# Performance work log

Measured on AMD Instinct MI355X. Metric: run time of the kernel, lower is better.

The kernel has to match this reference:

```python
import jax, jax.numpy as jnp
import numpy as np

N_NODES = 100000


def _sage_conv(x, src, dst, W_l, W_r, b):
    # mean aggregation of neighbor features over incoming edges (src -> dst)
    msgs = x[src]                                            # [E, d] gather
    agg = jax.ops.segment_sum(msgs, dst, num_segments=N_NODES)
    deg = jax.ops.segment_sum(jnp.ones_like(dst, dtype=x.dtype), dst,
                              num_segments=N_NODES)
    mean = agg / jnp.maximum(deg, 1.0)[:, None]              # [N, d]
    # PyG SAGEConv: lin_l(aggr) + lin_r(x); bias lives in lin_l
    return mean @ W_l + x @ W_r + b


def setup_inputs() -> dict:
    key = jax.random.key(0)
    k = jax.random.split(key, 8)
    d_in, d_h, E = 128, 128, 1600000
    scale_in = 1.0 / np.sqrt(d_in)
    scale_h = 1.0 / np.sqrt(d_h)
    return {
        "x": jax.random.normal(k[0], (N_NODES, d_in), dtype=jnp.float32),
        "edge_index": jax.random.randint(k[1], (2, E), 0, N_NODES, dtype=jnp.int64),
        "W_l0": jax.random.uniform(k[2], (d_in, d_h), jnp.float32, -scale_in, scale_in),
        "W_r0": jax.random.uniform(k[3], (d_in, d_h), jnp.float32, -scale_in, scale_in),
        "b0": jnp.zeros((d_h,), jnp.float32),
        "W_l1": jax.random.uniform(k[4], (d_h, d_h), jnp.float32, -scale_h, scale_h),
        "W_r1": jax.random.uniform(k[5], (d_h, d_h), jnp.float32, -scale_h, scale_h),
        "b1": jnp.zeros((d_h,), jnp.float32),
    }


def reference(x, edge_index, W_l0, W_r0, b0, W_l1, W_r1, b1):
    src, dst = edge_index[0], edge_index[1]
    h = _sage_conv(x, src, dst, W_l0, W_r0, b0)
    h = jax.nn.relu(h)  # dropout p=0.0 / eval mode -> identity
    h = _sage_conv(h, src, dst, W_l1, W_r1, b1)
    return h
```

## Files before the change

kernel.cpp:

```cpp
#include <hip/hip_runtime.h>


using bf16x8 = __attribute__((ext_vector_type(8))) __bf16;
using f32x4  = __attribute__((ext_vector_type(4))) float;
using f32x2  = __attribute__((ext_vector_type(2))) float;

__device__ __forceinline__ unsigned short f2bf(float f) {
    __bf16 b = (__bf16)f;
    return __builtin_bit_cast(unsigned short, b);
}
__device__ __forceinline__ unsigned pk2(float a, float b) {
    return (unsigned)f2bf(a) | ((unsigned)f2bf(b) << 16);
}

__device__ __forceinline__ int exscan1024(int v, int* wsum, int t) {
    int lane = t & 63, w = t >> 6;
    int x = v;
#pragma unroll
    for (int s = 1; s < 64; s <<= 1) {
        int y = __shfl_up(x, s);
        if (lane >= s) x += y;
    }
    if (lane == 63) wsum[w] = x;
    __syncthreads();
    if (w == 0) {
        int ws = (lane < 16) ? wsum[lane] : 0;
#pragma unroll
        for (int s = 1; s < 16; s <<= 1) {
            int y = __shfl_up(ws, s);
            if (lane >= s) ws += y;
        }
        if (lane < 16) wsum[lane] = ws;
    }
    __syncthreads();
    int base = (w > 0) ? wsum[w - 1] : 0;
    return base + x - v;
}


__global__ __launch_bounds__(256) void k_prep(
    const float4* __restrict__ x, uint4* __restrict__ xb8, int nvec, int ncvt,
    const float* __restrict__ W0, const float* __restrict__ W1,
    const float* __restrict__ W2, const float* __restrict__ W3,
    unsigned short* __restrict__ wsw, int ncvtw,
    const int* __restrict__ dst, int E, int* __restrict__ ghist, int nb, int nhist,
    int* __restrict__ gbase, int* __restrict__ gcur,
    int* __restrict__ row_start, int n)
{
    __shared__ int lh[800];
    const int b = blockIdx.x;
    if (b < ncvt) {
        int i = b * 256 + threadIdx.x;
        if (i >= nvec) return;
        float4 a = x[2 * i], c = x[2 * i + 1];
        uint4 o;
        o.x = pk2(a.x, a.y);
        o.y = pk2(a.z, a.w);
        o.z = pk2(c.x, c.y);
        o.w = pk2(c.z, c.w);
        xb8[i] = o;
    } else if (b < ncvt + ncvtw) {
        int id = (b - ncvt) * 256 + threadIdx.x;
        int m = id >> 14, r = id & 16383;
        int c = r >> 7, k = r & 127;
        const float* W = (m == 0) ? W0 : (m == 1) ? W1 : (m == 2) ? W2 : W3;
        wsw[m * 16384 + c * 128 + (k ^ ((c & 7) << 3))] = f2bf(W[k * 128 + c]);
    } else {
        int hb = b - ncvt - ncvtw;
        for (int i = threadIdx.x; i < nb; i += 256) lh[i] = 0;
        __syncthreads();
        for (int e = hb * 256 + threadIdx.x; e < E; e += nhist * 256)
            atomicAdd(&lh[dst[e] >> 7], 1);
        __syncthreads();
        for (int i = threadIdx.x; i < nb; i += 256)
            if (lh[i]) atomicAdd(&ghist[i], lh[i]);

        __shared__ int winflag;
        __shared__ int swsum[4];
        if (threadIdx.x == 0) {
            __threadfence();
            winflag = (atomicAdd(&ghist[nb], 1) == nhist - 1) ? 1 : 0;
        }
        __syncthreads();
        if (!winflag) return;
        __threadfence();

        const int t = threadIdx.x, lane = t & 63, w = t >> 6;
        const int i0 = t * 4;
        int v0 = (i0 + 0 < nb) ? __hip_atomic_load(&ghist[i0 + 0], __ATOMIC_RELAXED, __HIP_MEMORY_SCOPE_AGENT) : 0;
        int v1 = (i0 + 1 < nb) ? __hip_atomic_load(&ghist[i0 + 1], __ATOMIC_RELAXED, __HIP_MEMORY_SCOPE_AGENT) : 0;
        int v2 = (i0 + 2 < nb) ? __hip_atomic_load(&ghist[i0 + 2], __ATOMIC_RELAXED, __HIP_MEMORY_SCOPE_AGENT) : 0;
        int v3 = (i0 + 3 < nb) ? __hip_atomic_load(&ghist[i0 + 3], __ATOMIC_RELAXED, __HIP_MEMORY_SCOPE_AGENT) : 0;
        int s = v0 + v1 + v2 + v3;
        int xx = s;
#pragma unroll
        for (int sh = 1; sh < 64; sh <<= 1) {
            int y = __shfl_up(xx, sh);
            if (lane >= sh) xx += y;
        }
        if (lane == 63) swsum[w] = xx;
        __syncthreads();
        int base = 0;
        if (w > 0) base += swsum[0];
        if (w > 1) base += swsum[1];
        if (w > 2) base += swsum[2];
        int run = base + xx - s;
        if (i0 + 0 < nb) { gbase[i0 + 0] = run; gcur[i0 + 0] = run; } run += v0;
        if (i0 + 1 < nb) { gbase[i0 + 1] = run; gcur[i0 + 1] = run; } run += v1;
        if (i0 + 2 < nb) { gbase[i0 + 2] = run; gcur[i0 + 2] = run; } run += v2;
        if (i0 + 3 < nb) { gbase[i0 + 3] = run; gcur[i0 + 3] = run; }
        if (t == 0) { gbase[nb] = E; row_start[n] = E; }
    }
}


#define SC_CHUNK 8192

__global__ __launch_bounds__(1024) void k_binscatter(const int* __restrict__ src,
                                                     const int* __restrict__ dst, int E,
                                                     int* __restrict__ gcur,
                                                     unsigned* __restrict__ binned, int nb)
{
    __shared__ int lh[800];
    __shared__ int lbase[800];
    __shared__ int gb[800];
    __shared__ int wsum[16];
    __shared__ unsigned long long staged[SC_CHUNK];
    int t = threadIdx.x;
    int e0 = blockIdx.x * SC_CHUNK;
    if (e0 >= E) return;
    int ecnt = E - e0; if (ecnt > SC_CHUNK) ecnt = SC_CHUNK;

    for (int i = t; i < nb; i += 1024) lh[i] = 0;
    __syncthreads();
    for (int i = t; i < ecnt; i += 1024)
        atomicAdd(&lh[dst[e0 + i] >> 7], 1);
    __syncthreads();
    int v = (t < nb) ? lh[t] : 0;
    int excl = exscan1024(v, wsum, t);
    if (t < nb) {
        lbase[t] = excl;
        gb[t] = v ? atomicAdd(&gcur[t], v) : 0;
        lh[t] = excl;
    }
    __syncthreads();
    for (int i = t; i < ecnt; i += 1024) {
        int d = dst[e0 + i], s = src[e0 + i];
        int b = d >> 7;
        int rank = atomicAdd(&lh[b], 1);
        unsigned pack = ((unsigned)s << 7) | (unsigned)(d & 127);
        unsigned gaddr = (unsigned)gb[b] + (unsigned)(rank - lbase[b]);
        staged[rank] = ((unsigned long long)gaddr << 32) | pack;
    }
    __syncthreads();
    for (int i = t; i < ecnt; i += 1024) {
        unsigned long long w = staged[i];
        binned[(unsigned)(w >> 32)] = (unsigned)w;
    }
}


#define BS_STAGE 8192

__global__ __launch_bounds__(256) void k_bucketsort(
    const unsigned* __restrict__ binned,
    const int* __restrict__ gbase,
    int* __restrict__ csr,
    int* __restrict__ row_start,
    float* __restrict__ inv_deg,
    int n)
{
    __shared__ int cnt[128];
    __shared__ int cur[128];
    __shared__ int wsum[4];
    __shared__ unsigned stg[BS_STAGE];
    const int t = threadIdx.x;
    const int b = blockIdx.x;
    const int beg = gbase[b], end = gbase[b + 1];
    const int len = end - beg;

    if (t < 128) cnt[t] = 0;
    __syncthreads();
    for (int i = beg + t; i < end; i += 256)
        atomicAdd(&cnt[binned[i] & 127], 1);
    __syncthreads();
    int v = (t < 128) ? cnt[t] : 0;
    {
        int lane = t & 63, w = t >> 6;
        int x = v;
#pragma unroll
        for (int s = 1; s < 64; s <<= 1) {
            int y = __shfl_up(x, s);
            if (lane >= s) x += y;
        }
        if (lane == 63) wsum[w] = x;
        __syncthreads();
        int base = (w == 1) ? wsum[0] : (w == 2) ? wsum[0] + wsum[1]
                 : (w == 3) ? wsum[0] + wsum[1] + wsum[2] : 0;
        int excl = base + x - v;
        if (t < 128) {
            cur[t] = excl;
            int node = b * 128 + t;
            if (node < n) {
                row_start[node] = beg + excl;
                inv_deg[node] = 1.f / (float)max(v, 1);
            }
        }
    }
    __syncthreads();

    if (len <= BS_STAGE) {
        for (int i = beg + t; i < end; i += 256) {
            unsigned w = binned[i];
            int r = atomicAdd(&cur[w & 127], 1);
            stg[r] = w >> 7;
        }
        __syncthreads();
        for (int i = t; i < len; i += 256)
            csr[beg + i] = (int)stg[i];
    } else {
        for (int i = beg + t; i < end; i += 256) {
            unsigned w = binned[i];
            int r = atomicAdd(&cur[w & 127], 1);
            csr[beg + r] = (int)(w >> 7);
        }
    }
}


__device__ __forceinline__ f32x2 up2(unsigned x) {
    return (f32x2){__builtin_bit_cast(float, x << 16),
                   __builtin_bit_cast(float, x & 0xffff0000u)};
}
__device__ __forceinline__ void acc8(f32x2* a, uint4 v) {
    a[0] += up2(v.x);
    a[1] += up2(v.y);
    a[2] += up2(v.z);
    a[3] += up2(v.w);
}

__global__ __launch_bounds__(256) void k_agg(
    const unsigned short* __restrict__ feat,
    const int* __restrict__ csr,
    const int* __restrict__ row_start,
    const float* __restrict__ inv_deg,
    unsigned short* __restrict__ mean, int n)
{
    const int node = blockIdx.x * 4 + (threadIdx.x >> 6);
    if (node >= n) return;
    const int lane = threadIdx.x & 63;
    const int q  = lane >> 4;
    const int cg = (lane & 15) << 3;
    const unsigned short* fp = feat + cg;
    const int beg = row_start[node], end = row_start[node + 1];

    f32x2 a[4];
#pragma unroll
    for (int j = 0; j < 4; ++j) a[j] = (f32x2){0.f, 0.f};

    for (int i = beg; i < end; i += 64) {
        int cnt = end - i; if (cnt > 64) cnt = 64;
        const int lim = i + cnt - 1;
        for (int e = 0; e < cnt; e += 16) {
            int p0 = i + e + q;      p0 = p0 < lim ? p0 : lim;
            int p1 = i + e + 4 + q;  p1 = p1 < lim ? p1 : lim;
            int p2 = i + e + 8 + q;  p2 = p2 < lim ? p2 : lim;
            int p3 = i + e + 12 + q; p3 = p3 < lim ? p3 : lim;
            int s0 = csr[p0];
            int s1 = csr[p1];
            int s2 = csr[p2];
            int s3 = csr[p3];
            uint4 v0 = *(const uint4*)(fp + ((size_t)s0 << 7));
            uint4 v1 = *(const uint4*)(fp + ((size_t)s1 << 7));
            uint4 v2 = *(const uint4*)(fp + ((size_t)s2 << 7));
            uint4 v3 = *(const uint4*)(fp + ((size_t)s3 << 7));
            if (e + q      < cnt) acc8(a, v0);
            if (e + 4 + q  < cnt) acc8(a, v1);
            if (e + 8 + q  < cnt) acc8(a, v2);
            if (e + 12 + q < cnt) acc8(a, v3);
        }
    }

#pragma unroll
    for (int j = 0; j < 4; ++j) {
        a[j].x += __shfl_xor(a[j].x, 16);
        a[j].x += __shfl_xor(a[j].x, 32);
        a[j].y += __shfl_xor(a[j].y, 16);
        a[j].y += __shfl_xor(a[j].y, 32);
    }

    if (q == 0) {
        float w = inv_deg[node];
        uint4 o;
        o.x = pk2(a[0].x * w, a[0].y * w);
        o.y = pk2(a[1].x * w, a[1].y * w);
        o.z = pk2(a[2].x * w, a[2].y * w);
        o.w = pk2(a[3].x * w, a[3].y * w);
        *(uint4*)(mean + (size_t)node * 128 + cg) = o;
    }
}


template<bool RELU, bool OUTF32>
__global__ __launch_bounds__(256) void k_gemm(
    const unsigned short* __restrict__ A1,
    const unsigned short* __restrict__ A2,
    const unsigned short* __restrict__ Wsw,
    const float* __restrict__ bias,
    void* __restrict__ outv,
    int nrows)
{
    __shared__ __align__(16) unsigned short Wt[2 * 128 * 128];
    {
        const uint4* wsrc = (const uint4*)Wsw;
        uint4* wdst = (uint4*)Wt;
#pragma unroll
        for (int i = 0; i < 16; ++i)
            wdst[threadIdx.x + 256 * i] = wsrc[threadIdx.x + 256 * i];
    }
    __syncthreads();

    const int lane = threadIdx.x & 63;
    const int wave = threadIdx.x >> 6;
    const int lr = lane & 15;
    const int lg = lane >> 4;
    const int row0 = blockIdx.x * 128 + wave * 32;
    const int sw = (lr & 7) << 3;

    f32x4 acc[2][8];
#pragma unroll
    for (int m = 0; m < 2; ++m)
#pragma unroll
        for (int nn = 0; nn < 8; ++nn) acc[m][nn] = (f32x4){0.f, 0.f, 0.f, 0.f};

#pragma unroll
    for (int ks = 0; ks < 4; ++ks) {
        const int k0 = ks * 32 + lg * 8;
        bf16x8 a1[2], a2[2];
#pragma unroll
        for (int m = 0; m < 2; ++m) {
            int r = row0 + m * 16 + lr;
            if (r >= nrows) r = nrows - 1;
            a1[m] = *reinterpret_cast<const bf16x8*>(A1 + (size_t)r * 128 + k0);
            a2[m] = *reinterpret_cast<const bf16x8*>(A2 + (size_t)r * 128 + k0);
        }
        const int kidx = k0 ^ sw;
#pragma unroll
        for (int nn = 0; nn < 8; ++nn) {
            const int c = nn * 16 + lr;
            bf16x8 b1 = *reinterpret_cast<const bf16x8*>(&Wt[c * 128 + kidx]);
            bf16x8 b2 = *reinterpret_cast<const bf16x8*>(&Wt[16384 + c * 128 + kidx]);
#pragma unroll
            for (int m = 0; m < 2; ++m) {
                acc[m][nn] = __builtin_amdgcn_mfma_f32_16x16x32_bf16(a1[m], b1, acc[m][nn], 0, 0, 0);
                acc[m][nn] = __builtin_amdgcn_mfma_f32_16x16x32_bf16(a2[m], b2, acc[m][nn], 0, 0, 0);
            }
        }
    }

    __syncthreads();

#pragma unroll
    for (int m = 0; m < 2; ++m) {
#pragma unroll
        for (int nn = 0; nn < 8; ++nn) {
            const int c = nn * 16 + lr;
            const float bv = bias[c];
#pragma unroll
            for (int i = 0; i < 4; ++i) {
                int r = row0 + m * 16 + lg * 4 + i;
                if (r < nrows) {
                    float v = acc[m][nn][i] + bv;
                    if (RELU) v = fmaxf(v, 0.f);
                    if (OUTF32)
                        ((float*)outv)[(size_t)r * 128 + c] = v;
                    else
                        ((unsigned short*)outv)[(size_t)r * 128 + c] = f2bf(v);
                }
            }
        }
    }
}


extern "C" void kernel_launch(void* const* d_in, const int* in_sizes, int n_in,
                              void* d_out, int out_size, void* d_ws, size_t ws_size,
                              hipStream_t stream)
{
    const float* x   = (const float*)d_in[0];
    const int*   ei  = (const int*)d_in[1];
    const float* Wl0 = (const float*)d_in[2];
    const float* Wr0 = (const float*)d_in[3];
    const float* b0  = (const float*)d_in[4];
    const float* Wl1 = (const float*)d_in[5];
    const float* Wr1 = (const float*)d_in[6];
    const float* b1  = (const float*)d_in[7];
    float* out = (float*)d_out;

    const int n = in_sizes[0] / 128;
    const int E = in_sizes[1] / 2;
    const int* src = ei;
    const int* dst = ei + E;
    const int nb = (n + 127) >> 7;

    char* ws = (char*)d_ws;
    size_t off = 0;
    auto alloc = [&](size_t sz) -> char* {
        char* p = ws + off;
        off += (sz + 1023) & ~(size_t)1023;
        return p;
    };
    unsigned short* xb     = (unsigned short*)alloc((size_t)n * 128 * 2);
    unsigned short* mean   = (unsigned short*)alloc((size_t)n * 128 * 2);
    unsigned*       binned = (unsigned*)      alloc((size_t)E * 4);
    int*            rs     = (int*)           alloc((size_t)(n + 1) * 4);
    float*          invd   = (float*)         alloc((size_t)n * 4);
    int*            ghist  = (int*)           alloc((size_t)(nb + 1) * 4);
    int*            gbase  = (int*)           alloc((size_t)(nb + 1) * 4);
    int*            gcur   = (int*)           alloc((size_t)nb * 4);
    unsigned short* wsw    = (unsigned short*)alloc(4 * 16384 * 2);
    int* csr;
    if (off + (size_t)E * 4 <= ws_size) csr = (int*)alloc((size_t)E * 4);
    else                                csr = (int*)binned;
    if (ws_size < off) return;

    const int nvec  = n * 128 / 8;
    const int ncvt  = (nvec + 255) / 256;
    const int ncvtw = 256;
    const int nhist = 512;
    const int nsc   = (E + SC_CHUNK - 1) / SC_CHUNK;

    hipMemsetAsync(ghist, 0, (size_t)(nb + 1) * sizeof(int), stream);
    hipLaunchKernelGGL(k_prep, dim3(ncvt + ncvtw + nhist), dim3(256), 0, stream,
                       (const float4*)x, (uint4*)xb, nvec, ncvt,
                       Wl0, Wr0, Wl1, Wr1, wsw, ncvtw,
                       dst, E, ghist, nb, nhist,
                       gbase, gcur, rs, n);
    hipLaunchKernelGGL(k_binscatter, dim3(nsc),  dim3(1024), 0, stream,
                       src, dst, E, gcur, binned, nb);
    hipLaunchKernelGGL(k_bucketsort, dim3(nb),   dim3(256),  0, stream,
                       binned, gbase, csr, rs, invd, n);
    hipLaunchKernelGGL(k_agg,  dim3((n + 3) / 4), dim3(256), 0, stream,
                       xb, csr, rs, invd, mean, n);
    hipLaunchKernelGGL((k_gemm<true, false>), dim3(nb), dim3(256), 0, stream,
                       mean, xb, wsw, b0, (void*)xb, n);
    hipLaunchKernelGGL(k_agg,  dim3((n + 3) / 4), dim3(256), 0, stream,
                       xb, csr, rs, invd, mean, n);
    hipLaunchKernelGGL((k_gemm<false, true>), dim3(nb), dim3(256), 0, stream,
                       mean, xb, wsw + 2 * 16384, b1, (void*)out, n);
}
```

Measured before the change: 235.9 us.

## Fuse neighbor mean aggregation with SAGE GEMM per 128-node block

Merges the aggregation and GEMM kernels into one: each block aggregates 128 nodes into a swizzled LDS tile, then runs the MFMA GEMM straight from LDS. This drops the global round trip of the mean buffer and two launches. Edge indices are now loaded once per 64-edge chunk and broadcast with shuffles, and the weights are read from global/L2 instead of being staged in LDS. The cost is far fewer blocks for the gather phase (782 blocks of 4 waves, each wave walking 32 nodes one after another), which may hurt latency hiding. The layer-1 output also moves to a separate buffer.

```diff
diff --git a/kernel.cpp b/kernel.cpp
--- a/kernel.cpp
+++ b/kernel.cpp
@@ -239,93 +239,79 @@
     a[3] += up2(v.w);
 }
 
-__global__ __launch_bounds__(256) void k_agg(
+template<bool RELU, bool OUTF32>
+__global__ __launch_bounds__(256) void k_fused(
     const unsigned short* __restrict__ feat,
     const int* __restrict__ csr,
     const int* __restrict__ row_start,
     const float* __restrict__ inv_deg,
-    unsigned short* __restrict__ mean, int n)
-{
-    const int node = blockIdx.x * 4 + (threadIdx.x >> 6);
-    if (node >= n) return;
-    const int lane = threadIdx.x & 63;
-    const int q  = lane >> 4;
-    const int cg = (lane & 15) << 3;
-    const unsigned short* fp = feat + cg;
-    const int beg = row_start[node], end = row_start[node + 1];
-
-    f32x2 a[4];
-#pragma unroll
-    for (int j = 0; j < 4; ++j) a[j] = (f32x2){0.f, 0.f};
-
-    for (int i = beg; i < end; i += 64) {
-        int cnt = end - i; if (cnt > 64) cnt = 64;
-        const int lim = i + cnt - 1;
-        for (int e = 0; e < cnt; e += 16) {
-            int p0 = i + e + q;      p0 = p0 < lim ? p0 : lim;
-            int p1 = i + e + 4 + q;  p1 = p1 < lim ? p1 : lim;
-            int p2 = i + e + 8 + q;  p2 = p2 < lim ? p2 : lim;
-            int p3 = i + e + 12 + q; p3 = p3 < lim ? p3 : lim;
-            int s0 = csr[p0];
-            int s1 = csr[p1];
-            int s2 = csr[p2];
-            int s3 = csr[p3];
-            uint4 v0 = *(const uint4*)(fp + ((size_t)s0 << 7));
-            uint4 v1 = *(const uint4*)(fp + ((size_t)s1 << 7));
-            uint4 v2 = *(const uint4*)(fp + ((size_t)s2 << 7));
-            uint4 v3 = *(const uint4*)(fp + ((size_t)s3 << 7));
-            if (e + q      < cnt) acc8(a, v0);
-            if (e + 4 + q  < cnt) acc8(a, v1);
-            if (e + 8 + q  < cnt) acc8(a, v2);
-            if (e + 12 + q < cnt) acc8(a, v3);
-        }
-    }
-
-#pragma unroll
-    for (int j = 0; j < 4; ++j) {
-        a[j].x += __shfl_xor(a[j].x, 16);
-        a[j].x += __shfl_xor(a[j].x, 32);
-        a[j].y += __shfl_xor(a[j].y, 16);
-        a[j].y += __shfl_xor(a[j].y, 32);
-    }
-
-    if (q == 0) {
-        float w = inv_deg[node];
-        uint4 o;
-        o.x = pk2(a[0].x * w, a[0].y * w);
-        o.y = pk2(a[1].x * w, a[1].y * w);
-        o.z = pk2(a[2].x * w, a[2].y * w);
-        o.w = pk2(a[3].x * w, a[3].y * w);
-        *(uint4*)(mean + (size_t)node * 128 + cg) = o;
-    }
-}
-
-
-template<bool RELU, bool OUTF32>
-__global__ __launch_bounds__(256) void k_gemm(
-    const unsigned short* __restrict__ A1,
-    const unsigned short* __restrict__ A2,
     const unsigned short* __restrict__ Wsw,
     const float* __restrict__ bias,
     void* __restrict__ outv,
-    int nrows)
+    int n)
 {
-    __shared__ __align__(16) unsigned short Wt[2 * 128 * 128];
-    {
-        const uint4* wsrc = (const uint4*)Wsw;
-        uint4* wdst = (uint4*)Wt;
-#pragma unroll
-        for (int i = 0; i < 16; ++i)
-            wdst[threadIdx.x + 256 * i] = wsrc[threadIdx.x + 256 * i];
-    }
-    __syncthreads();
-
+    __shared__ __align__(16) unsigned short Ml[128 * 128];
     const int lane = threadIdx.x & 63;
     const int wave = threadIdx.x >> 6;
+    const int node0 = blockIdx.x * 128;
+
+    {
+        const int q  = lane >> 4;
+        const int cg = (lane & 15) << 3;
+        const unsigned short* fp = feat + cg;
+        for (int j = 0; j < 32; ++j) {
+            const int nl = wave * 32 + j;
+            const int node = node0 + nl;
+            f32x2 a[4];
+#pragma unroll
+            for (int k = 0; k < 4; ++k) a[k] = (f32x2){0.f, 0.f};
+            if (node < n) {
+                const int beg = row_start[node], end = row_start[node + 1];
+                for (int i = beg; i < end; i += 64) {
+                    int cnt = end - i; if (cnt > 64) cnt = 64;
+                    int idx = csr[i + (lane < cnt ? lane : cnt - 1)];
+                    for (int e = 0; e < cnt; e += 16) {
+                        const int r0 = e + q, r1 = e + 4 + q,
+                                  r2 = e + 8 + q, r3 = e + 12 + q;
+                        int s0 = __shfl(idx, r0 < cnt ? r0 : cnt - 1);
+                        int s1 = __shfl(idx, r1 < cnt ? r1 : cnt - 1);
+                        int s2 = __shfl(idx, r2 < cnt ? r2 : cnt - 1);
+                        int s3 = __shfl(idx, r3 < cnt ? r3 : cnt - 1);
+                        uint4 v0 = *(const uint4*)(fp + ((size_t)s0 << 7));
+                        uint4 v1 = *(const uint4*)(fp + ((size_t)s1 << 7));
+                        uint4 v2 = *(const uint4*)(fp + ((size_t)s2 << 7));
+                        uint4 v3 = *(const uint4*)(fp + ((size_t)s3 << 7));
+                        if (r0 < cnt) acc8(a, v0);
+                        if (r1 < cnt) acc8(a, v1);
+                        if (r2 < cnt) acc8(a, v2);
+                        if (r3 < cnt) acc8(a, v3);
+                    }
+                }
+            }
+#pragma unroll
+            for (int k = 0; k < 4; ++k) {
+                a[k].x += __shfl_xor(a[k].x, 16);
+                a[k].x += __shfl_xor(a[k].x, 32);
+                a[k].y += __shfl_xor(a[k].y, 16);
+                a[k].y += __shfl_xor(a[k].y, 32);
+            }
+            if (q == 0) {
+                float w = (node < n) ? inv_deg[node] : 0.f;
+                uint4 o;
+                o.x = pk2(a[0].x * w, a[0].y * w);
+                o.y = pk2(a[1].x * w, a[1].y * w);
+                o.z = pk2(a[2].x * w, a[2].y * w);
+                o.w = pk2(a[3].x * w, a[3].y * w);
+                *(uint4*)(&Ml[nl * 128 + (cg ^ ((nl & 7) << 3))]) = o;
+            }
+        }
+    }
+    __syncthreads();
+
     const int lr = lane & 15;
     const int lg = lane >> 4;
-    const int row0 = blockIdx.x * 128 + wave * 32;
     const int sw = (lr & 7) << 3;
+    const int row0l = wave * 32;
 
     f32x4 acc[2][8];
 #pragma unroll
@@ -339,17 +325,19 @@
         bf16x8 a1[2], a2[2];
 #pragma unroll
         for (int m = 0; m < 2; ++m) {
-            int r = row0 + m * 16 + lr;
-            if (r >= nrows) r = nrows - 1;
-            a1[m] = *reinterpret_cast<const bf16x8*>(A1 + (size_t)r * 128 + k0);
-            a2[m] = *reinterpret_cast<const bf16x8*>(A2 + (size_t)r * 128 + k0);
+            const int rl = row0l + m * 16 + lr;
+            a1[m] = *reinterpret_cast<const bf16x8*>(
+                        &Ml[rl * 128 + (k0 ^ ((rl & 7) << 3))]);
+            int r = node0 + rl;
+            if (r >= n) r = n - 1;
+            a2[m] = *reinterpret_cast<const bf16x8*>(feat + (size_t)r * 128 + k0);
         }
         const int kidx = k0 ^ sw;
 #pragma unroll
         for (int nn = 0; nn < 8; ++nn) {
             const int c = nn * 16 + lr;
-            bf16x8 b1 = *reinterpret_cast<const bf16x8*>(&Wt[c * 128 + kidx]);
-            bf16x8 b2 = *reinterpret_cast<const bf16x8*>(&Wt[16384 + c * 128 + kidx]);
+            bf16x8 b1 = *reinterpret_cast<const bf16x8*>(Wsw + c * 128 + kidx);
+            bf16x8 b2 = *reinterpret_cast<const bf16x8*>(Wsw + 16384 + c * 128 + kidx);
 #pragma unroll
             for (int m = 0; m < 2; ++m) {
                 acc[m][nn] = __builtin_amdgcn_mfma_f32_16x16x32_bf16(a1[m], b1, acc[m][nn], 0, 0, 0);
@@ -358,8 +346,6 @@
         }
     }
 
-    __syncthreads();
-
 #pragma unroll
     for (int m = 0; m < 2; ++m) {
 #pragma unroll
@@ -368,8 +354,8 @@
             const float bv = bias[c];
 #pragma unroll
             for (int i = 0; i < 4; ++i) {
-                int r = row0 + m * 16 + lg * 4 + i;
-                if (r < nrows) {
+                int r = node0 + row0l + m * 16 + lg * 4 + i;
+                if (r < n) {
                     float v = acc[m][nn][i] + bv;
                     if (RELU) v = fmaxf(v, 0.f);
                     if (OUTF32)
@@ -411,7 +397,7 @@
         return p;
     };
     unsigned short* xb     = (unsigned short*)alloc((size_t)n * 128 * 2);
-    unsigned short* mean   = (unsigned short*)alloc((size_t)n * 128 * 2);
+    unsigned short* hbuf   = (unsigned short*)alloc((size_t)n * 128 * 2);
     unsigned*       binned = (unsigned*)      alloc((size_t)E * 4);
     int*            rs     = (int*)           alloc((size_t)(n + 1) * 4);
     float*          invd   = (float*)         alloc((size_t)n * 4);
@@ -440,12 +426,8 @@
                        src, dst, E, gcur, binned, nb);
     hipLaunchKernelGGL(k_bucketsort, dim3(nb),   dim3(256),  0, stream,
                        binned, gbase, csr, rs, invd, n);
-    hipLaunchKernelGGL(k_agg,  dim3((n + 3) / 4), dim3(256), 0, stream,
-                       xb, csr, rs, invd, mean, n);
-    hipLaunchKernelGGL((k_gemm<true, false>), dim3(nb), dim3(256), 0, stream,
-                       mean, xb, wsw, b0, (void*)xb, n);
-    hipLaunchKernelGGL(k_agg,  dim3((n + 3) / 4), dim3(256), 0, stream,
-                       xb, csr, rs, invd, mean, n);
-    hipLaunchKernelGGL((k_gemm<false, true>), dim3(nb), dim3(256), 0, stream,
-                       mean, xb, wsw + 2 * 16384, b1, (void*)out, n);
-}
+    hipLaunchKernelGGL((k_fused<true, false>), dim3(nb), dim3(256), 0, stream,
+                       xb, csr, rs, invd, wsw, b0, (void*)hbuf, n);
+    hipLaunchKernelGGL((k_fused<false, true>), dim3(nb), dim3(256), 0, stream,
+                       hbuf, csr, rs, invd, wsw + 2 * 16384, b1, (void*)out, n);
+}
```

Result: slower. 372.7 us (+58.0%).
